# Performance work log

Measured on AMD Instinct MI355X. Metric: run time of the kernel, lower is better.

Reference implementation:

```python
import jax, jax.numpy as jnp
import numpy as np
from jax.ops import segment_sum, segment_max

N = 50000
E = 800000
IN_C, HID_C, OUT_C, HEADS = 64, 128, 32, 4
BN_EPS = 1e-5
NEG_SLOPE = 0.2


def setup_inputs() -> dict:
    key = jax.random.key(0)
    ks = jax.random.split(key, 16)
    s = 0.1  # weight scale for numerical sanity
    inp = {
        'x': jax.random.normal(ks[0], (N, IN_C), jnp.float32),
        'edge_index': jax.random.randint(ks[1], (2, E), 0, N, jnp.int64),
        'sage1_wl': jax.random.normal(ks[2], (IN_C, HID_C), jnp.float32) * s,
        'sage1_bl': jnp.zeros((HID_C,), jnp.float32),
        'sage1_wr': jax.random.normal(ks[3], (IN_C, HID_C), jnp.float32) * s,
        'bn1_gamma': jnp.ones((HID_C,), jnp.float32),
        'bn1_beta': jnp.zeros((HID_C,), jnp.float32),
        'bn1_mean': jnp.zeros((HID_C,), jnp.float32),
        'bn1_var': jnp.ones((HID_C,), jnp.float32),
        'sage2_wl': jax.random.normal(ks[4], (HID_C, HID_C), jnp.float32) * s,
        'sage2_bl': jnp.zeros((HID_C,), jnp.float32),
        'sage2_wr': jax.random.normal(ks[5], (HID_C, HID_C), jnp.float32) * s,
        'bn2_gamma': jnp.ones((HID_C,), jnp.float32),
        'bn2_beta': jnp.zeros((HID_C,), jnp.float32),
        'bn2_mean': jnp.zeros((HID_C,), jnp.float32),
        'bn2_var': jnp.ones((HID_C,), jnp.float32),
        'gat_w': jax.random.normal(ks[6], (HID_C, HEADS * OUT_C), jnp.float32) * s,
        'gat_att_src': jax.random.normal(ks[7], (HEADS, OUT_C), jnp.float32) * s,
        'gat_att_dst': jax.random.normal(ks[8], (HEADS, OUT_C), jnp.float32) * s,
        'gat_bias': jnp.zeros((OUT_C,), jnp.float32),
        'cls_w1': jax.random.normal(ks[9], (OUT_C, 64), jnp.float32) * s,
        'cls_b1': jnp.zeros((64,), jnp.float32),
        'cls_w2': jax.random.normal(ks[10], (64, 1), jnp.float32) * s,
        'cls_b2': jnp.zeros((1,), jnp.float32),
    }
    return inp


def _sage_conv(x, src, dst, n, wl, bl, wr):
    # PyG SAGEConv (mean aggr): lin_l(mean_{j in N(i)} x_j) + lin_r(x_i)
    agg = segment_sum(x[src], dst, num_segments=n)           # [N, C]
    cnt = segment_sum(jnp.ones((src.shape[0], 1), x.dtype), dst, num_segments=n)
    mean = agg / jnp.maximum(cnt, 1.0)
    return mean @ wl + bl + x @ wr


def _bn_eval(x, gamma, beta, mean, var):
    return (x - mean) * jax.lax.rsqrt(var + BN_EPS) * gamma + beta


def _gat_conv(x, src, dst, n, w, att_src, att_dst, bias):
    # PyG GATConv, concat=False (head-average), add_self_loops=True
    loop = jnp.arange(n, dtype=src.dtype)
    s = jnp.concatenate([src, loop])
    d = jnp.concatenate([dst, loop])
    h = (x @ w).reshape(n, HEADS, OUT_C)                     # [N, H, C]
    a_src = jnp.einsum('nhc,hc->nh', h, att_src)             # [N, H]
    a_dst = jnp.einsum('nhc,hc->nh', h, att_dst)             # [N, H]
    e = jax.nn.leaky_relu(a_src[s] + a_dst[d], NEG_SLOPE)    # [Etot, H]
    m = segment_max(e, d, num_segments=n)                    # stable softmax per dst
    ex = jnp.exp(e - m[d])
    den = segment_sum(ex, d, num_segments=n)
    alpha = ex / den[d]                                      # [Etot, H]
    out = segment_sum(alpha[:, :, None] * h[s], d, num_segments=n)  # [N, H, C]
    return out.mean(axis=1) + bias                           # concat=False -> mean over heads


def reference(x, edge_index,
              sage1_wl, sage1_bl, sage1_wr,
              bn1_gamma, bn1_beta, bn1_mean, bn1_var,
              sage2_wl, sage2_bl, sage2_wr,
              bn2_gamma, bn2_beta, bn2_mean, bn2_var,
              gat_w, gat_att_src, gat_att_dst, gat_bias,
              cls_w1, cls_b1, cls_w2, cls_b2):
    n = x.shape[0]
    src, dst = edge_index[0], edge_index[1]
    # Layer 0: SAGE(64->128) + BN + ReLU (no residual: shapes differ); dropout = eval noop
    h = _sage_conv(x, src, dst, n, sage1_wl, sage1_bl, sage1_wr)
    h = jax.nn.relu(_bn_eval(h, bn1_gamma, bn1_beta, bn1_mean, bn1_var))
    # Layer 1: SAGE(128->128) + BN + residual + ReLU
    identity = h
    h2 = _sage_conv(h, src, dst, n, sage2_wl, sage2_bl, sage2_wr)
    h2 = _bn_eval(h2, bn2_gamma, bn2_beta, bn2_mean, bn2_var) + identity
    h2 = jax.nn.relu(h2)
    # Final layer: GAT head (128 -> 32, 4 heads averaged)
    embeddings = _gat_conv(h2, src, dst, n, gat_w, gat_att_src, gat_att_dst, gat_bias)
    # MLP classifier (dropout eval noop)
    logits = jax.nn.relu(embeddings @ cls_w1 + cls_b1) @ cls_w2 + cls_b2
    return embeddings, logits
```

## Files before the change

### kernel.cpp

```cpp
#include <hip/hip_runtime.h>

typedef unsigned int uint_t;
typedef unsigned short ush;
typedef short bf16x8 __attribute__((ext_vector_type(8)));
typedef float f32x4 __attribute__((ext_vector_type(4)));

constexpr int TPB = 256;
#define LOG2E 1.4426950408889634f

__device__ __forceinline__ float lrelu(float x){ return fmaxf(x, 0.f) + 0.2f*fminf(x, 0.f); }
__device__ __forceinline__ ush f2b(float f){
  uint_t u = __float_as_uint(f);
  return (ush)((u + 0x7fffu + ((u >> 16) & 1u)) >> 16);
}
__device__ __forceinline__ float b2f(ush s){ return __uint_as_float(((uint_t)s) << 16); }
__device__ __forceinline__ float blo(uint_t u){ return __uint_as_float(u << 16); }
__device__ __forceinline__ float bhi(uint_t u){ return __uint_as_float(u & 0xffff0000u); }

__global__ void k_bnfold(const float* __restrict__ g1, const float* __restrict__ b1,
                         const float* __restrict__ m1, const float* __restrict__ v1,
                         const float* __restrict__ g2, const float* __restrict__ b2,
                         const float* __restrict__ m2, const float* __restrict__ v2,
                         float* __restrict__ out){
  int t = threadIdx.x;
  int o = t & 127;
  bool second = t >= 128;
  const float* g = second ? g2 : g1;  const float* b = second ? b2 : b1;
  const float* m = second ? m2 : m1;  const float* v = second ? v2 : v1;
  float sc = g[o] * rsqrtf(v[o] + 1e-5f);
  float sh = b[o] - m[o]*sc;
  int off = second ? 256 : 0;
  out[off + o] = sc;
  out[off + 128 + o] = sh;
}

__global__ void k_deg(const int* __restrict__ dst, int* __restrict__ degi, int E){
  int t = blockIdx.x*TPB + threadIdx.x;
  if (t < E) atomicAdd(&degi[dst[t]], 1);
}

__global__ __launch_bounds__(1024) void k_scan1(const int* __restrict__ deg,
                                                int* __restrict__ out,
                                                int* __restrict__ bsum, int n){
  __shared__ int ws[16];
  int tid = threadIdx.x;
  int gid = blockIdx.x*1024 + tid;
  int v = (gid < n) ? deg[gid] : 0;
  int lane = tid & 63, wid = tid >> 6;
  int s = v;
  for (int off = 1; off < 64; off <<= 1){
    int t2 = __shfl_up(s, off);
    if (lane >= off) s += t2;
  }
  if (lane == 63) ws[wid] = s;
  __syncthreads();
  if (wid == 0){
    int w = (lane < 16) ? ws[lane] : 0;
    for (int off = 1; off < 16; off <<= 1){
      int t2 = __shfl_up(w, off);
      if (lane >= off) w += t2;
    }
    if (lane < 16) ws[lane] = w;
  }
  __syncthreads();
  int base = wid > 0 ? ws[wid-1] : 0;
  int incl = base + s;
  if (gid < n) out[gid] = incl - v;
  if (tid == 1023) bsum[blockIdx.x] = incl;
}

__global__ void k_scan2(int* __restrict__ bsum, int nb){
  int lane = threadIdx.x;
  int carry = 0;
  for (int base = 0; base < nb; base += 64){
    int i = base + lane;
    int v = (i < nb) ? bsum[i] : 0;
    int s = v;
    for (int off = 1; off < 64; off <<= 1){
      int t2 = __shfl_up(s, off);
      if (lane >= off) s += t2;
    }
    if (i < nb) bsum[i] = carry + s - v;
    int tot = __shfl(s, 63);
    carry += tot;
  }
  if (lane == 0) bsum[nb] = carry;
}

__global__ void k_scan3(int* __restrict__ offs, const int* __restrict__ bsum, int n, int nb){
  int gid = blockIdx.x*TPB + threadIdx.x;
  if (gid < n) offs[gid] += bsum[gid >> 10];
  else if (gid == n) offs[n] = bsum[nb];
}

__global__ void k_fill(const int* __restrict__ src, const int* __restrict__ dst,
                       const int* __restrict__ offs, int* __restrict__ cur,
                       int* __restrict__ esrc, int* __restrict__ edst, int E){
  int t = blockIdx.x*TPB + threadIdx.x;
  if (t >= E) return;
  int d = dst[t];
  int p = offs[d] + atomicAdd(&cur[d], 1);
  esrc[p] = src[t];
  edst[p] = d;
}

__global__ void k_tobf16(const float* __restrict__ in, ush* __restrict__ out, int n4){
  int t = blockIdx.x*TPB + threadIdx.x;
  if (t >= n4) return;
  float4 v = *(const float4*)(in + (size_t)t*4);
  ushort4 o;
  o.x = f2b(v.x); o.y = f2b(v.y); o.z = f2b(v.z); o.w = f2b(v.w);
  *(ushort4*)(out + (size_t)t*4) = o;
}

__global__ void k_wprep(const float* __restrict__ wr, const float* __restrict__ wl,
                        int C1, int K, ush* __restrict__ WT){
  int t = blockIdx.x*TPB + threadIdx.x;
  if (t >= 128*K) return;
  int n = t / K, k = t % K;
  float v = (k < C1) ? wr[(size_t)k*128 + n] : wl[(size_t)(k - C1)*128 + n];
  WT[t] = f2b(v);
}

template<int C>
__global__ __launch_bounds__(256) void k_gather_mean_b(
    const int* __restrict__ offs, const int* __restrict__ esrc,
    const uint_t* __restrict__ xb, uint_t* __restrict__ meanb, int n){
  constexpr int L = C/2;
  int tid = threadIdx.x;
  int nid = blockIdx.x*(256/L) + tid/L;
  int l = tid % L;
  if (nid >= n) return;
  int k0 = offs[nid], k1 = offs[nid+1];
  const int* sp = esrc + k0;
  int cnt = k1 - k0;
  float s0 = 0.f, s1 = 0.f;
  int k = 0;
  for (; k + 8 <= cnt; k += 8){
    int e0 = sp[k],   e1 = sp[k+1], e2 = sp[k+2], e3 = sp[k+3];
    int e4 = sp[k+4], e5 = sp[k+5], e6 = sp[k+6], e7 = sp[k+7];
    uint_t u0 = xb[(size_t)e0*L + l];
    uint_t u1 = xb[(size_t)e1*L + l];
    uint_t u2 = xb[(size_t)e2*L + l];
    uint_t u3 = xb[(size_t)e3*L + l];
    uint_t u4 = xb[(size_t)e4*L + l];
    uint_t u5 = xb[(size_t)e5*L + l];
    uint_t u6 = xb[(size_t)e6*L + l];
    uint_t u7 = xb[(size_t)e7*L + l];
    s0 += ((blo(u0) + blo(u1)) + (blo(u2) + blo(u3)))
        + ((blo(u4) + blo(u5)) + (blo(u6) + blo(u7)));
    s1 += ((bhi(u0) + bhi(u1)) + (bhi(u2) + bhi(u3)))
        + ((bhi(u4) + bhi(u5)) + (bhi(u6) + bhi(u7)));
  }
  for (; k + 4 <= cnt; k += 4){
    int e0 = sp[k], e1 = sp[k+1], e2 = sp[k+2], e3 = sp[k+3];
    uint_t u0 = xb[(size_t)e0*L + l];
    uint_t u1 = xb[(size_t)e1*L + l];
    uint_t u2 = xb[(size_t)e2*L + l];
    uint_t u3 = xb[(size_t)e3*L + l];
    s0 += (blo(u0) + blo(u1)) + (blo(u2) + blo(u3));
    s1 += (bhi(u0) + bhi(u1)) + (bhi(u2) + bhi(u3));
  }
  for (; k < cnt; ++k){
    uint_t u = xb[(size_t)sp[k]*L + l];
    s0 += blo(u);
    s1 += bhi(u);
  }
  float inv = 1.f / (float)max(cnt, 1);
  uint_t lo = f2b(s0*inv), hi = f2b(s1*inv);
  meanb[(size_t)nid*L + l] = lo | (hi << 16);
}

template<int K, bool BN, bool RES, bool RELU>
__global__ __launch_bounds__(256) void k_mm_mfma(
    const ush* __restrict__ A1, int C1,
    const ush* __restrict__ A2,
    const ush* __restrict__ WT,
    const float* __restrict__ bias,
    const float* __restrict__ bnp, int bnoff,
    const float* __restrict__ res,
    float* __restrict__ out, ush* __restrict__ outb, int n)
{
  constexpr int PAD = K + 8;
  __shared__ ush sA[32][PAD];
  int tid = threadIdx.x;
  int wave = tid >> 6, lane = tid & 63;
  int node0 = blockIdx.x * 32;
  int C2 = K - C1;

  for (int idx = tid; idx < 32*(K/8); idx += 256) {
    int r  = idx / (K/8);
    int kc = (idx % (K/8)) * 8;
    int g = node0 + r;
    uint4 v = make_uint4(0,0,0,0);
    if (g < n) {
      if (kc < C1) v = *(const uint4*)(A1 + (size_t)g*C1 + kc);
      else         v = *(const uint4*)(A2 + (size_t)g*C2 + (kc - C1));
    }
    *(uint4*)&sA[r][kc] = v;
  }
  __syncthreads();

  f32x4 acc[2][2] = {};
  int l15 = lane & 15, lk = (lane >> 4) * 8;
  const ush* wt0 = WT + (size_t)(wave*32 + l15) * K + lk;
  const ush* wt1 = wt0 + (size_t)16 * K;

  #pragma unroll
  for (int kk = 0; kk < K; kk += 32) {
    bf16x8 a0 = *(const bf16x8*)&sA[l15][kk + lk];
    bf16x8 a1 = *(const bf16x8*)&sA[16 + l15][kk + lk];
    bf16x8 b0 = *(const bf16x8*)(wt0 + kk);
    bf16x8 b1 = *(const bf16x8*)(wt1 + kk);
    acc[0][0] = __builtin_amdgcn_mfma_f32_16x16x32_bf16(a0, b0, acc[0][0], 0, 0, 0);
    acc[0][1] = __builtin_amdgcn_mfma_f32_16x16x32_bf16(a0, b1, acc[0][1], 0, 0, 0);
    acc[1][0] = __builtin_amdgcn_mfma_f32_16x16x32_bf16(a1, b0, acc[1][0], 0, 0, 0);
    acc[1][1] = __builtin_amdgcn_mfma_f32_16x16x32_bf16(a1, b1, acc[1][1], 0, 0, 0);
  }

  int r0 = (lane >> 4) * 4;
  #pragma unroll
  for (int mt = 0; mt < 2; ++mt) {
    #pragma unroll
    for (int nt = 0; nt < 2; ++nt) {
      int nn = wave*32 + nt*16 + l15;
      float bv = bias ? bias[nn] : 0.f;
      float sc = 1.f, sh = 0.f;
      if constexpr (BN) { sc = bnp[bnoff + nn]; sh = bnp[bnoff + 128 + nn]; }
      #pragma unroll
      for (int j = 0; j < 4; ++j) {
        int g = node0 + mt*16 + r0 + j;
        if (g < n) {
          float v = acc[mt][nt][j] + bv;
          if constexpr (BN)   v = v*sc + sh;
          if constexpr (RES)  v += res[(size_t)g*128 + nn];
          if constexpr (RELU) v = fmaxf(v, 0.f);
          if (out)  out[(size_t)g*128 + nn] = v;
          if (outb) outb[(size_t)g*128 + nn] = f2b(v);
        }
      }
    }
  }
}

__global__ void k_attn(const uint_t* __restrict__ hgb, const float* __restrict__ atts,
                       const float* __restrict__ attd, float* __restrict__ asrc,
                       float* __restrict__ adst, int n){
  int t = blockIdx.x*TPB + threadIdx.x;
  if (t >= n*4) return;
  int nid = t >> 2, h = t & 3;
  const uint_t* hp = hgb + (size_t)nid*64 + h*16;
  float as = 0.f, ad = 0.f;
  #pragma unroll
  for (int i = 0; i < 16; ++i) {
    uint_t u = hp[i];
    float v0 = blo(u);
    float v1 = bhi(u);
    as = fmaf(v0, atts[h*32 + 2*i],     as);
    as = fmaf(v1, atts[h*32 + 2*i + 1], as);
    ad = fmaf(v0, attd[h*32 + 2*i],     ad);
    ad = fmaf(v1, attd[h*32 + 2*i + 1], ad);
  }
  asrc[t] = as * LOG2E; adst[t] = ad * LOG2E;
}

__global__ void k_eexp(const int* __restrict__ esrc, const int* __restrict__ edst,
                       const float* __restrict__ asrc, const float* __restrict__ adst,
                       float* __restrict__ exf, int E4){
  int t = blockIdx.x*TPB + threadIdx.x;
  if (t >= E4) return;
  int k = t >> 2, h = t & 3;
  int s = esrc[k], d = edst[k];
  exf[t] = exp2f(lrelu(asrc[s*4 + h] + adst[d*4 + h]));
}

__global__ __launch_bounds__(256) void k_gat(
    const int* __restrict__ offs, const int* __restrict__ esrc,
    const float* __restrict__ exf,
    const float* __restrict__ asrc, const float* __restrict__ adst,
    const uint_t* __restrict__ hgb, const float* __restrict__ gbias,
    const float* __restrict__ w1, const float* __restrict__ b1,
    const float* __restrict__ w2, const float* __restrict__ b2,
    float* __restrict__ out_emb, float* __restrict__ out_log, int n){
  __shared__ float semb[4][32];
  int tid = threadIdx.x;
  int wl = tid >> 6;
  int l = tid & 63;
  int nid = blockIdx.x*4 + wl;
  if (nid >= n) return;
  int h = l >> 4;
  int i4 = nid*4 + h;
  float e0 = exp2f(lrelu(asrc[i4] + adst[i4]));
  uint_t u = hgb[(size_t)nid*64 + l];
  float accD  = e0;
  float accN0 = e0 * blo(u);
  float accN1 = e0 * bhi(u);
  int k0 = offs[nid], k1 = offs[nid+1];
  const int* sp = esrc + k0;
  const float* ep = exf + (size_t)k0*4 + h;
  int cnt = k1 - k0;
  int k = 0;
  for (; k + 8 <= cnt; k += 8){
    int s0 = sp[k],   s1 = sp[k+1], s2 = sp[k+2], s3 = sp[k+3];
    int s4 = sp[k+4], s5 = sp[k+5], s6 = sp[k+6], s7 = sp[k+7];
    float e0_ = ep[4*k],    e1_ = ep[4*k+4],  e2_ = ep[4*k+8],  e3_ = ep[4*k+12];
    float e4_ = ep[4*k+16], e5_ = ep[4*k+20], e6_ = ep[4*k+24], e7_ = ep[4*k+28];
    uint_t v0 = hgb[(size_t)s0*64 + l];
    uint_t v1 = hgb[(size_t)s1*64 + l];
    uint_t v2 = hgb[(size_t)s2*64 + l];
    uint_t v3 = hgb[(size_t)s3*64 + l];
    uint_t v4 = hgb[(size_t)s4*64 + l];
    uint_t v5 = hgb[(size_t)s5*64 + l];
    uint_t v6 = hgb[(size_t)s6*64 + l];
    uint_t v7 = hgb[(size_t)s7*64 + l];
    accD += ((e0_ + e1_) + (e2_ + e3_)) + ((e4_ + e5_) + (e6_ + e7_));
    accN0 = fmaf(e0_, blo(v0), accN0);
    accN0 = fmaf(e1_, blo(v1), accN0);
    accN0 = fmaf(e2_, blo(v2), accN0);
    accN0 = fmaf(e3_, blo(v3), accN0);
    accN0 = fmaf(e4_, blo(v4), accN0);
    accN0 = fmaf(e5_, blo(v5), accN0);
    accN0 = fmaf(e6_, blo(v6), accN0);
    accN0 = fmaf(e7_, blo(v7), accN0);
    accN1 = fmaf(e0_, bhi(v0), accN1);
    accN1 = fmaf(e1_, bhi(v1), accN1);
    accN1 = fmaf(e2_, bhi(v2), accN1);
    accN1 = fmaf(e3_, bhi(v3), accN1);
    accN1 = fmaf(e4_, bhi(v4), accN1);
    accN1 = fmaf(e5_, bhi(v5), accN1);
    accN1 = fmaf(e6_, bhi(v6), accN1);
    accN1 = fmaf(e7_, bhi(v7), accN1);
  }
  for (; k + 4 <= cnt; k += 4){
    int s0 = sp[k], s1 = sp[k+1], s2 = sp[k+2], s3 = sp[k+3];
    float e0_ = ep[4*k], e1_ = ep[4*k+4], e2_ = ep[4*k+8], e3_ = ep[4*k+12];
    uint_t v0 = hgb[(size_t)s0*64 + l];
    uint_t v1 = hgb[(size_t)s1*64 + l];
    uint_t v2 = hgb[(size_t)s2*64 + l];
    uint_t v3 = hgb[(size_t)s3*64 + l];
    accD += (e0_ + e1_) + (e2_ + e3_);
    accN0 = fmaf(e0_, blo(v0), accN0);
    accN0 = fmaf(e1_, blo(v1), accN0);
    accN0 = fmaf(e2_, blo(v2), accN0);
    accN0 = fmaf(e3_, blo(v3), accN0);
    accN1 = fmaf(e0_, bhi(v0), accN1);
    accN1 = fmaf(e1_, bhi(v1), accN1);
    accN1 = fmaf(e2_, bhi(v2), accN1);
    accN1 = fmaf(e3_, bhi(v3), accN1);
  }
  for (; k < cnt; ++k){
    float e = ep[4*k];
    uint_t v = hgb[(size_t)sp[k]*64 + l];
    accD += e;
    accN0 = fmaf(e, blo(v), accN0);
    accN1 = fmaf(e, bhi(v), accN1);
  }
  float inv = 1.f / accD;
  float v0 = accN0 * inv, v1 = accN1 * inv;
  v0 += __shfl_xor(v0, 16); v0 += __shfl_xor(v0, 32);
  v1 += __shfl_xor(v1, 16); v1 += __shfl_xor(v1, 32);
  if (l < 16){
    int c = l*2;
    float2 o;
    o.x = 0.25f*v0 + gbias[c];
    o.y = 0.25f*v1 + gbias[c+1];
    *(float2*)(out_emb + (size_t)nid*32 + c) = o;
    semb[wl][c] = o.x;
    semb[wl][c+1] = o.y;
  }
  float a = b1[l];
  #pragma unroll
  for (int c = 0; c < 32; ++c) a = fmaf(semb[wl][c], w1[c*64 + l], a);
  float t = fmaxf(a, 0.f) * w2[l];
  t += __shfl_xor(t, 1);  t += __shfl_xor(t, 2);  t += __shfl_xor(t, 4);
  t += __shfl_xor(t, 8);  t += __shfl_xor(t, 16); t += __shfl_xor(t, 32);
  if (l == 0) out_log[nid] = t + b2[0];
}

extern "C" void kernel_launch(void* const* d_in, const int* in_sizes, int n_in,
                              void* d_out, int out_size, void* d_ws, size_t ws_size,
                              hipStream_t stream) {
  const float* x    = (const float*)d_in[0];
  const int*   ei   = (const int*)  d_in[1];
  const float* s1wl = (const float*)d_in[2];
  const float* s1bl = (const float*)d_in[3];
  const float* s1wr = (const float*)d_in[4];
  const float* bn1g = (const float*)d_in[5];
  const float* bn1b = (const float*)d_in[6];
  const float* bn1m = (const float*)d_in[7];
  const float* bn1v = (const float*)d_in[8];
  const float* s2wl = (const float*)d_in[9];
  const float* s2bl = (const float*)d_in[10];
  const float* s2wr = (const float*)d_in[11];
  const float* bn2g = (const float*)d_in[12];
  const float* bn2b = (const float*)d_in[13];
  const float* bn2m = (const float*)d_in[14];
  const float* bn2v = (const float*)d_in[15];
  const float* gatw = (const float*)d_in[16];
  const float* atts = (const float*)d_in[17];
  const float* attd = (const float*)d_in[18];
  const float* gatb = (const float*)d_in[19];
  const float* cw1  = (const float*)d_in[20];
  const float* cb1  = (const float*)d_in[21];
  const float* cw2  = (const float*)d_in[22];
  const float* cb2  = (const float*)d_in[23];

  const int N = in_sizes[0] / 64;
  const int E = in_sizes[1] / 2;
  const int* src = ei;
  const int* dst = ei + E;
  const int NBK = (N + 1023) / 1024;

  float* h1   = (float*)d_ws;
  float* asrc = h1 + (size_t)N*128;
  float* adst = asrc + (size_t)N*4;
  float* bnp  = adst + (size_t)N*4;
  ush* regA = (ush*)(bnp + 512);
  ush* regB = regA + (size_t)N*128;
  ush* regC = regB + (size_t)N*128;
  ush* W1T  = regC + (size_t)N*128;
  ush* W2T  = W1T + 128*128;
  ush* WGT  = W2T + 128*256;
  int* degi = (int*)(WGT + 128*128);
  int* offs = degi + N;
  int* cur  = offs + N + 1;
  int* esrc = cur + N;
  int* edst = esrc + E;
  int* bsum = edst + E;

  ush* xb     = regA;
  ush* mean1b = regA + (size_t)N*64;
  ush* mean2b = regA;
  ush* h1b    = regB;
  ush* hgb    = regB;
  ush* h2b    = regC;
  float* exf  = h1;

  float* out_emb = (float*)d_out;
  float* out_log = out_emb + (size_t)N*32;

  hipMemsetAsync(degi, 0, (size_t)N*4, stream);
  hipMemsetAsync(cur,  0, (size_t)N*4, stream);

  k_bnfold<<<1, 256, 0, stream>>>(bn1g,bn1b,bn1m,bn1v, bn2g,bn2b,bn2m,bn2v, bnp);

  k_deg<<<(E+TPB-1)/TPB, TPB, 0, stream>>>(dst, degi, E);
  k_scan1<<<NBK, 1024, 0, stream>>>(degi, offs, bsum, N);
  k_scan2<<<1, 64, 0, stream>>>(bsum, NBK);
  k_scan3<<<(N+1+TPB-1)/TPB, TPB, 0, stream>>>(offs, bsum, N, NBK);
  k_fill<<<(E+TPB-1)/TPB, TPB, 0, stream>>>(src, dst, offs, cur, esrc, edst, E);

  k_wprep<<<(128*128+TPB-1)/TPB, TPB, 0, stream>>>(s1wr, s1wl, 64, 128, W1T);
  k_wprep<<<(128*256+TPB-1)/TPB, TPB, 0, stream>>>(s2wr, s2wl, 128, 256, W2T);
  k_wprep<<<(128*128+TPB-1)/TPB, TPB, 0, stream>>>(gatw, nullptr, 128, 128, WGT);

  k_tobf16<<<(N*16+TPB-1)/TPB, TPB, 0, stream>>>(x, xb, N*16);

  int nmm = (N + 31) / 32;

  k_gather_mean_b<64><<<(N+7)/8, 256, 0, stream>>>(offs, esrc, (const uint_t*)xb, (uint_t*)mean1b, N);
  k_mm_mfma<128,true,false,true><<<nmm, 256, 0, stream>>>(
      xb, 64, mean1b, W1T, s1bl, bnp, 0, nullptr, h1, h1b, N);

  k_gather_mean_b<128><<<(N+3)/4, 256, 0, stream>>>(offs, esrc, (const uint_t*)h1b, (uint_t*)mean2b, N);
  k_mm_mfma<256,true,true,true><<<nmm, 256, 0, stream>>>(
      h1b, 128, mean2b, W2T, s2bl, bnp, 256, h1, nullptr, h2b, N);

  k_mm_mfma<128,false,false,false><<<nmm, 256, 0, stream>>>(
      h2b, 128, nullptr, WGT, nullptr, bnp, 0, nullptr, nullptr, hgb, N);

  k_attn<<<(N*4+TPB-1)/TPB, TPB, 0, stream>>>((const uint_t*)hgb, atts, attd, asrc, adst, N);
  k_eexp<<<(E*4+TPB-1)/TPB, TPB, 0, stream>>>(esrc, edst, asrc, adst, exf, E*4);
  k_gat<<<(N+3)/4, 256, 0, stream>>>(offs, esrc, exf, asrc, adst, (const uint_t*)hgb, gatb,
                                     cw1, cb1, cw2, cb2, out_emb, out_log, N);
}
```

Measured before the change: 298.0 us.

## Fuse GAT edge attention exponent into aggregation kernel and drop edst array

Removes the separate per-edge exp kernel and the stored exf buffer. The aggregation kernel now computes each edge's attention weight on the fly: lanes split a 16-edge chunk, each computes one exp2 for its head, and the values are broadcast with shuffles. The edst write in CSR fill is removed because nothing reads it any more. This saves one launch and the write and re-read of a 12.8MB per-edge buffer, at the cost of extra shuffles and gathers of asrc inside the aggregation loop.

```diff
diff --git a/kernel.cpp b/kernel.cpp
--- a/kernel.cpp
+++ b/kernel.cpp
@@ -95,13 +95,12 @@
 
 __global__ void k_fill(const int* __restrict__ src, const int* __restrict__ dst,
                        const int* __restrict__ offs, int* __restrict__ cur,
-                       int* __restrict__ esrc, int* __restrict__ edst, int E){
+                       int* __restrict__ esrc, int E){
   int t = blockIdx.x*TPB + threadIdx.x;
   if (t >= E) return;
   int d = dst[t];
   int p = offs[d] + atomicAdd(&cur[d], 1);
   esrc[p] = src[t];
-  edst[p] = d;
 }
 
 __global__ void k_tobf16(const float* __restrict__ in, ush* __restrict__ out, int n4){
@@ -264,19 +263,8 @@
   asrc[t] = as * LOG2E; adst[t] = ad * LOG2E;
 }
 
-__global__ void k_eexp(const int* __restrict__ esrc, const int* __restrict__ edst,
-                       const float* __restrict__ asrc, const float* __restrict__ adst,
-                       float* __restrict__ exf, int E4){
-  int t = blockIdx.x*TPB + threadIdx.x;
-  if (t >= E4) return;
-  int k = t >> 2, h = t & 3;
-  int s = esrc[k], d = edst[k];
-  exf[t] = exp2f(lrelu(asrc[s*4 + h] + adst[d*4 + h]));
-}
-
 __global__ __launch_bounds__(256) void k_gat(
     const int* __restrict__ offs, const int* __restrict__ esrc,
-    const float* __restrict__ exf,
     const float* __restrict__ asrc, const float* __restrict__ adst,
     const uint_t* __restrict__ hgb, const float* __restrict__ gbias,
     const float* __restrict__ w1, const float* __restrict__ b1,
@@ -289,68 +277,50 @@
   int nid = blockIdx.x*4 + wl;
   if (nid >= n) return;
   int h = l >> 4;
+  int j16 = l & 15;
+  int hb = l & 48;
   int i4 = nid*4 + h;
-  float e0 = exp2f(lrelu(asrc[i4] + adst[i4]));
+  float ad = adst[i4];
+  float e0 = exp2f(lrelu(asrc[i4] + ad));
   uint_t u = hgb[(size_t)nid*64 + l];
   float accD  = e0;
   float accN0 = e0 * blo(u);
   float accN1 = e0 * bhi(u);
   int k0 = offs[nid], k1 = offs[nid+1];
   const int* sp = esrc + k0;
-  const float* ep = exf + (size_t)k0*4 + h;
   int cnt = k1 - k0;
   int k = 0;
-  for (; k + 8 <= cnt; k += 8){
-    int s0 = sp[k],   s1 = sp[k+1], s2 = sp[k+2], s3 = sp[k+3];
-    int s4 = sp[k+4], s5 = sp[k+5], s6 = sp[k+6], s7 = sp[k+7];
-    float e0_ = ep[4*k],    e1_ = ep[4*k+4],  e2_ = ep[4*k+8],  e3_ = ep[4*k+12];
-    float e4_ = ep[4*k+16], e5_ = ep[4*k+20], e6_ = ep[4*k+24], e7_ = ep[4*k+28];
-    uint_t v0 = hgb[(size_t)s0*64 + l];
-    uint_t v1 = hgb[(size_t)s1*64 + l];
-    uint_t v2 = hgb[(size_t)s2*64 + l];
-    uint_t v3 = hgb[(size_t)s3*64 + l];
-    uint_t v4 = hgb[(size_t)s4*64 + l];
-    uint_t v5 = hgb[(size_t)s5*64 + l];
-    uint_t v6 = hgb[(size_t)s6*64 + l];
-    uint_t v7 = hgb[(size_t)s7*64 + l];
-    accD += ((e0_ + e1_) + (e2_ + e3_)) + ((e4_ + e5_) + (e6_ + e7_));
-    accN0 = fmaf(e0_, blo(v0), accN0);
-    accN0 = fmaf(e1_, blo(v1), accN0);
-    accN0 = fmaf(e2_, blo(v2), accN0);
-    accN0 = fmaf(e3_, blo(v3), accN0);
-    accN0 = fmaf(e4_, blo(v4), accN0);
-    accN0 = fmaf(e5_, blo(v5), accN0);
-    accN0 = fmaf(e6_, blo(v6), accN0);
-    accN0 = fmaf(e7_, blo(v7), accN0);
-    accN1 = fmaf(e0_, bhi(v0), accN1);
-    accN1 = fmaf(e1_, bhi(v1), accN1);
-    accN1 = fmaf(e2_, bhi(v2), accN1);
-    accN1 = fmaf(e3_, bhi(v3), accN1);
-    accN1 = fmaf(e4_, bhi(v4), accN1);
-    accN1 = fmaf(e5_, bhi(v5), accN1);
-    accN1 = fmaf(e6_, bhi(v6), accN1);
-    accN1 = fmaf(e7_, bhi(v7), accN1);
-  }
-  for (; k + 4 <= cnt; k += 4){
-    int s0 = sp[k], s1 = sp[k+1], s2 = sp[k+2], s3 = sp[k+3];
-    float e0_ = ep[4*k], e1_ = ep[4*k+4], e2_ = ep[4*k+8], e3_ = ep[4*k+12];
-    uint_t v0 = hgb[(size_t)s0*64 + l];
-    uint_t v1 = hgb[(size_t)s1*64 + l];
-    uint_t v2 = hgb[(size_t)s2*64 + l];
-    uint_t v3 = hgb[(size_t)s3*64 + l];
-    accD += (e0_ + e1_) + (e2_ + e3_);
-    accN0 = fmaf(e0_, blo(v0), accN0);
-    accN0 = fmaf(e1_, blo(v1), accN0);
-    accN0 = fmaf(e2_, blo(v2), accN0);
-    accN0 = fmaf(e3_, blo(v3), accN0);
-    accN1 = fmaf(e0_, bhi(v0), accN1);
-    accN1 = fmaf(e1_, bhi(v1), accN1);
-    accN1 = fmaf(e2_, bhi(v2), accN1);
-    accN1 = fmaf(e3_, bhi(v3), accN1);
+  for (; k + 16 <= cnt; k += 16){
+    int mys = sp[k + j16];
+    float mye = exp2f(lrelu(asrc[mys*4 + h] + ad));
+    #pragma unroll
+    for (int j = 0; j < 16; ++j){
+      float e = __shfl(mye, hb | j);
+      int s   = sp[k + j];
+      uint_t v = hgb[(size_t)s*64 + l];
+      accD += e;
+      accN0 = fmaf(e, blo(v), accN0);
+      accN1 = fmaf(e, bhi(v), accN1);
+    }
+  }
+  if (k + 8 <= cnt){
+    int mys = sp[k + (j16 & 7)];
+    float mye = exp2f(lrelu(asrc[mys*4 + h] + ad));
+    #pragma unroll
+    for (int j = 0; j < 8; ++j){
+      float e = __shfl(mye, hb | j);
+      int s   = sp[k + j];
+      uint_t v = hgb[(size_t)s*64 + l];
+      accD += e;
+      accN0 = fmaf(e, blo(v), accN0);
+      accN1 = fmaf(e, bhi(v), accN1);
+    }
+    k += 8;
   }
   for (; k < cnt; ++k){
-    float e = ep[4*k];
-    uint_t v = hgb[(size_t)sp[k]*64 + l];
+    int s = sp[k];
+    float e = exp2f(lrelu(asrc[s*4 + h] + ad));
+    uint_t v = hgb[(size_t)s*64 + l];
     accD += e;
     accN0 = fmaf(e, blo(v), accN0);
     accN1 = fmaf(e, bhi(v), accN1);
@@ -425,8 +395,7 @@
   int* offs = degi + N;
   int* cur  = offs + N + 1;
   int* esrc = cur + N;
-  int* edst = esrc + E;
-  int* bsum = edst + E;
+  int* bsum = esrc + E;
 
   ush* xb     = regA;
   ush* mean1b = regA + (size_t)N*64;
@@ -434,7 +403,6 @@
   ush* h1b    = regB;
   ush* hgb    = regB;
   ush* h2b    = regC;
-  float* exf  = h1;
 
   float* out_emb = (float*)d_out;
   float* out_log = out_emb + (size_t)N*32;
@@ -448,7 +416,7 @@
   k_scan1<<<NBK, 1024, 0, stream>>>(degi, offs, bsum, N);
   k_scan2<<<1, 64, 0, stream>>>(bsum, NBK);
   k_scan3<<<(N+1+TPB-1)/TPB, TPB, 0, stream>>>(offs, bsum, N, NBK);
-  k_fill<<<(E+TPB-1)/TPB, TPB, 0, stream>>>(src, dst, offs, cur, esrc, edst, E);
+  k_fill<<<(E+TPB-1)/TPB, TPB, 0, stream>>>(src, dst, offs, cur, esrc, E);
 
   k_wprep<<<(128*128+TPB-1)/TPB, TPB, 0, stream>>>(s1wr, s1wl, 64, 128, W1T);
   k_wprep<<<(128*256+TPB-1)/TPB, TPB, 0, stream>>>(s2wr, s2wl, 128, 256, W2T);
@@ -470,7 +438,6 @@
       h2b, 128, nullptr, WGT, nullptr, bnp, 0, nullptr, nullptr, hgb, N);
 
   k_attn<<<(N*4+TPB-1)/TPB, TPB, 0, stream>>>((const uint_t*)hgb, atts, attd, asrc, adst, N);
-  k_eexp<<<(E*4+TPB-1)/TPB, TPB, 0, stream>>>(esrc, edst, asrc, adst, exf, E*4);
-  k_gat<<<(N+3)/4, 256, 0, stream>>>(offs, esrc, exf, asrc, adst, (const uint_t*)hgb, gatb,
+  k_gat<<<(N+3)/4, 256, 0, stream>>>(offs, esrc, asrc, adst, (const uint_t*)hgb, gatb,
                                      cw1, cb1, cw2, cb2, out_emb, out_log, N);
 }
```

New measurement: 294.1 us. Within noise of the previous version (-1.3%).
